# Optimization experiments

Measured on AMD Instinct MI355X. Metric: run time of the kernel, lower is better.

Reference implementation:

```python
import jax, jax.numpy as jnp
import numpy as np

D_MODEL = 512
D_INNER = 2 * D_MODEL      # 1024
DT_RANK = D_MODEL // 16    # 32
D_STATE = 16
D_CONV = 4
NB_LAYERS = 3
BATCH = 64
SEQ = 201
CITY = 200
EPS = 1e-5


def setup_inputs() -> dict:
    key = jax.random.key(0)
    ks = jax.random.split(key, 12)
    def rn(k, shape, scale=0.02):
        return jax.random.normal(k, shape, jnp.float32) * scale
    A_init = jnp.tile(jnp.arange(1, D_STATE + 1, dtype=jnp.float32)[None, None, :],
                      (NB_LAYERS, D_INNER, 1))
    return {
        "x": jax.random.uniform(ks[0], (BATCH, SEQ, 2), jnp.float32),
        "city_count": CITY,
        "embed_W": rn(ks[1], (D_MODEL, 2), 0.5),
        "embed_b": jnp.zeros((D_MODEL,), jnp.float32),
        "norm_w": jnp.ones((NB_LAYERS, D_MODEL), jnp.float32),
        "norm_b": jnp.zeros((NB_LAYERS, D_MODEL), jnp.float32),
        "in_W": rn(ks[2], (NB_LAYERS, 2 * D_INNER, D_MODEL)),
        "conv_w": rn(ks[3], (NB_LAYERS, D_INNER, D_CONV), 0.1),
        "conv_b": jnp.zeros((NB_LAYERS, D_INNER), jnp.float32),
        "xproj_W": rn(ks[4], (NB_LAYERS, DT_RANK + 2 * D_STATE, D_INNER)),
        "dtproj_W": rn(ks[5], (NB_LAYERS, D_INNER, DT_RANK), 0.1),
        "dtproj_b": rn(ks[6], (NB_LAYERS, D_INNER), 0.5),
        "A_log": jnp.log(A_init),
        "Dskip": jnp.ones((NB_LAYERS, D_INNER), jnp.float32),
        "out_W": rn(ks[7], (NB_LAYERS, D_MODEL, D_INNER)),
        "normf_w": jnp.ones((D_MODEL,), jnp.float32),
        "normf_b": jnp.zeros((D_MODEL,), jnp.float32),
        "head_W": rn(ks[8], (CITY, D_MODEL)),
    }


def _silu(v):
    return v * jax.nn.sigmoid(v)


def _layernorm(v, w, b):
    v = v.astype(jnp.float32)
    mu = v.mean(-1, keepdims=True)
    var = ((v - mu) ** 2).mean(-1, keepdims=True)
    return (v - mu) * jax.lax.rsqrt(var + EPS) * w + b


def _rmsnorm(v, w, b):
    v = v.astype(jnp.float32)
    ms = (v * v).mean(-1, keepdims=True)
    return v * jax.lax.rsqrt(ms + EPS) * w + b


def _mamba_mixer(h, in_W, cw, cb, xp_W, dt_W, dt_b, A_log, Dv, o_W):
    B, L, _ = h.shape
    xz = jnp.einsum('bld,ed->ble', h, in_W)              # (B,L,2*di)
    xc, z = jnp.split(xz, 2, axis=-1)
    # causal depthwise conv over time
    xt = xc.transpose(0, 2, 1)                           # (B,di,L)
    xt = jax.lax.conv_general_dilated(
        xt, cw[:, None, :], (1,), [(D_CONV - 1, 0)],
        dimension_numbers=('NCH', 'OIH', 'NCH'),
        feature_group_count=D_INNER)
    u = _silu((xt + cb[None, :, None]).transpose(0, 2, 1))   # (B,L,di)
    x_dbl = jnp.einsum('bld,ed->ble', u, xp_W)
    dt_r = x_dbl[..., :DT_RANK]
    Bm = x_dbl[..., DT_RANK:DT_RANK + D_STATE]
    Cm = x_dbl[..., DT_RANK + D_STATE:]
    dt = jax.nn.softplus(jnp.einsum('blr,dr->bld', dt_r, dt_W) + dt_b)
    A = -jnp.exp(A_log)                                  # (di,n)

    def step(hst, ins):
        dt_t, B_t, C_t, u_t = ins                        # (B,di),(B,n),(B,n),(B,di)
        dA = jnp.exp(dt_t[..., None] * A)                # (B,di,n)
        hst = dA * hst + (dt_t * u_t)[..., None] * B_t[:, None, :]
        y = jnp.einsum('bdn,bn->bd', hst, C_t)
        return hst, y

    h0 = jnp.zeros((B, D_INNER, D_STATE), h.dtype)
    _, ys = jax.lax.scan(step, h0, (dt.transpose(1, 0, 2), Bm.transpose(1, 0, 2),
                                    Cm.transpose(1, 0, 2), u.transpose(1, 0, 2)))
    y = ys.transpose(1, 0, 2) + Dv * u
    y = y * _silu(z)
    return jnp.einsum('bld,ed->ble', y, o_W)


def reference(x, city_count, embed_W, embed_b, norm_w, norm_b, in_W, conv_w, conv_b,
              xproj_W, dtproj_W, dtproj_b, A_log, Dskip, out_W, normf_w, normf_b, head_W):
    h = jnp.einsum('blc,dc->bld', x, embed_W) + embed_b
    residual = None
    for i in range(NB_LAYERS):
        residual = h if residual is None else h + residual   # residual in fp32
        hn = _layernorm(residual, norm_w[i], norm_b[i])
        h = _mamba_mixer(hn, in_W[i], conv_w[i], conv_b[i], xproj_W[i],
                         dtproj_W[i], dtproj_b[i], A_log[i], Dskip[i], out_W[i])
    residual = h + residual
    xf = _rmsnorm(residual, normf_w, normf_b)                # final fused RMSNorm
    logits = jnp.einsum('bld,cd->blc', xf, head_W)           # output head -> city logits
    return logits
```

## Files before the change

### kernel.cpp

```cpp
#include <hip/hip_runtime.h>
#include <hip/hip_fp16.h>
#include <math.h>

#define D_MODEL 512
#define D_INNER 1024
#define DT_RANK 32
#define D_STATE 16
#define D_CONV 4
#define NB_LAYERS 3
#define BATCH 64
#define SEQ 201
#define CITY 200
#define M_ROWS (BATCH * SEQ)
#define M_PAD 12928
#define EPS 1e-5f
#define NCH 8
#define CL 26

typedef __attribute__((ext_vector_type(8))) short short8;
typedef __attribute__((ext_vector_type(8))) unsigned short ushort8;
typedef __attribute__((ext_vector_type(4))) float f32x4;

__device__ __forceinline__ float sigmoidf_(float x) { return 1.f / (1.f + __expf(-x)); }

__device__ __forceinline__ unsigned short f2b(float f) {
  union { float f; unsigned int u; } v; v.f = f;
  unsigned int r = (v.u + 0x7fff + ((v.u >> 16) & 1)) >> 16;
  return (unsigned short)r;
}
__device__ __forceinline__ float b2f(unsigned short h) {
  union { unsigned int u; float f; } v; v.u = ((unsigned int)h) << 16; return v.f;
}
__device__ __forceinline__ unsigned short f2h(float f) {
  __half h = __float2half(f); return *(unsigned short*)&h;
}
__device__ __forceinline__ float h2f(unsigned short u) {
  __half h = *(__half*)&u; return __half2float(h);
}

__device__ __forceinline__ void gload_lds16(const void* g, void* l) {
  __builtin_amdgcn_global_load_lds(
      (const __attribute__((address_space(1))) void*)g,
      (__attribute__((address_space(3))) void*)l, 16, 0, 0);
}

__global__ __launch_bounds__(256) void k_f2b(const float* __restrict__ in,
                                             unsigned short* __restrict__ out,
                                             int n, int n_total) {
  int i = blockIdx.x * 256 + threadIdx.x;
  if (i < n) out[i] = f2b(in[i]);
  else if (i < n_total) out[i] = 0;
}

__global__ __launch_bounds__(256) void k_padW(const float* __restrict__ W,
                                              unsigned short* __restrict__ out,
                                              int rows, int incols, int outcols) {
  int i = blockIdx.x * 256 + threadIdx.x;
  if (i >= rows * outcols) return;
  int n = i / outcols, k = i - n * outcols;
  out[i] = (k < incols) ? f2b(W[(size_t)n * incols + k]) : 0;
}

__global__ __launch_bounds__(256) void k_padR(const float* __restrict__ W,
                                              unsigned short* __restrict__ out,
                                              int nl, int inrows, int outrows, int cols) {
  int i = blockIdx.x * 256 + threadIdx.x;
  if (i >= nl * outrows * cols) return;
  int c = i % cols;
  int r = (i / cols) % outrows;
  int L = i / (cols * outrows);
  out[i] = (r < inrows) ? f2b(W[((size_t)L * inrows + r) * cols + c]) : 0;
}

__global__ __launch_bounds__(256) void k_convT(const float* __restrict__ cw,
                                               float* __restrict__ cwT) {
  int i = blockIdx.x * 256 + threadIdx.x;
  if (i >= NB_LAYERS * D_CONV * D_INNER) return;
  int d = i & (D_INNER - 1);
  int k = (i >> 10) & 3;
  int L = i >> 12;
  cwT[i] = cw[((size_t)L * D_INNER + d) * D_CONV + k];
}

__global__ __launch_bounds__(256) void k_embed(const float* __restrict__ x,
                                               const float* __restrict__ W,
                                               const float* __restrict__ b,
                                               float* __restrict__ h) {
  int idx = blockIdx.x * 256 + threadIdx.x;
  if (idx >= M_ROWS * D_MODEL) return;
  int d = idx & (D_MODEL - 1);
  int m = idx >> 9;
  float x0 = x[m * 2 + 0], x1 = x[m * 2 + 1];
  h[idx] = fmaf(x0, W[d * 2 + 0], fmaf(x1, W[d * 2 + 1], b[d]));
}

__global__ __launch_bounds__(256) void k_resid_norm(const float* __restrict__ h,
                                                    float* __restrict__ resid,
                                                    float* __restrict__ out,
                                                    unsigned short* __restrict__ out_b,
                                                    const float* __restrict__ w,
                                                    const float* __restrict__ b,
                                                    int addRes, int mode) {
  int row = blockIdx.x * 4 + (threadIdx.x >> 6);
  int lane = threadIdx.x & 63;
  if (row >= M_ROWS) return;
  const float* hp = h + (size_t)row * D_MODEL;
  float* rp = resid + (size_t)row * D_MODEL;
  float v[8];
#pragma unroll
  for (int j = 0; j < 8; ++j) {
    float t = hp[j * 64 + lane];
    if (addRes) t += rp[j * 64 + lane];
    v[j] = t;
    rp[j * 64 + lane] = t;
  }
  float mu = 0.f, rstd;
  if (mode == 0) {
    float s = 0.f;
#pragma unroll
    for (int j = 0; j < 8; ++j) s += v[j];
#pragma unroll
    for (int o = 1; o < 64; o <<= 1) s += __shfl_xor(s, o);
    mu = s * (1.f / D_MODEL);
    float vs = 0.f;
#pragma unroll
    for (int j = 0; j < 8; ++j) { float d0 = v[j] - mu; vs += d0 * d0; }
#pragma unroll
    for (int o = 1; o < 64; o <<= 1) vs += __shfl_xor(vs, o);
    rstd = rsqrtf(vs * (1.f / D_MODEL) + EPS);
  } else {
    float s = 0.f;
#pragma unroll
    for (int j = 0; j < 8; ++j) s += v[j] * v[j];
#pragma unroll
    for (int o = 1; o < 64; o <<= 1) s += __shfl_xor(s, o);
    rstd = rsqrtf(s * (1.f / D_MODEL) + EPS);
  }
#pragma unroll
  for (int j = 0; j < 8; ++j) {
    int c = j * 64 + lane;
    float o = (v[j] - mu) * rstd * w[c] + b[c];
    if (out) out[(size_t)row * D_MODEL + c] = o;
    if (out_b) out_b[(size_t)row * D_MODEL + c] = f2b(o);
  }
}

template <int BOUT, int ACT>
__global__ __launch_bounds__(256) void k_gemm_mfma(const unsigned short* __restrict__ A,
                                                   const unsigned short* __restrict__ B,
                                                   const float* __restrict__ bias,
                                                   void* __restrict__ Cv, int ldc,
                                                   int M, int Nout, int K) {
  __shared__ unsigned short lA[2][128 * 64];
  __shared__ unsigned short lB[2][128 * 64];
  int tid = threadIdx.x;
  int wave = tid >> 6, lane = tid & 63;
  int bm = blockIdx.y * 128, bn = blockIdx.x * 128;
  int wm = (wave >> 1) * 64, wn = (wave & 1) * 64;
  f32x4 acc[4][4] = {};

  auto stage = [&](int kt, int bb) {
    int k0 = kt * 64;
#pragma unroll
    for (int i = 0; i < 4; ++i) {
      int e = (i * 256 + tid) * 8;
      int r = e >> 6, c = e & 63;
      gload_lds16(A + (size_t)(bm + r) * K + k0 + c, &lA[bb][e]);
      gload_lds16(B + (size_t)(bn + r) * K + k0 + c, &lB[bb][e]);
    }
  };

  int nk = K >> 6;
  stage(0, 0);
  __syncthreads();
  for (int t = 0; t < nk; ++t) {
    int cur = t & 1;
    if (t + 1 < nk) stage(t + 1, cur ^ 1);
#pragma unroll
    for (int ks = 0; ks < 2; ++ks) {
      int koff = ks * 32 + (lane >> 4) * 8;
      short8 a[4], b[4];
#pragma unroll
      for (int i = 0; i < 4; ++i)
        a[i] = *(const short8*)&lA[cur][(wm + i * 16 + (lane & 15)) * 64 + koff];
#pragma unroll
      for (int j = 0; j < 4; ++j)
        b[j] = *(const short8*)&lB[cur][(wn + j * 16 + (lane & 15)) * 64 + koff];
#pragma unroll
      for (int i = 0; i < 4; ++i)
#pragma unroll
        for (int j = 0; j < 4; ++j)
          acc[i][j] = __builtin_amdgcn_mfma_f32_16x16x32_bf16(a[i], b[j], acc[i][j], 0, 0, 0);
    }
    __syncthreads();
  }
#pragma unroll
  for (int i = 0; i < 4; ++i) {
    int row0 = bm + wm + i * 16 + (lane >> 4) * 4;
#pragma unroll
    for (int j = 0; j < 4; ++j) {
      int col = bn + wn + j * 16 + (lane & 15);
#pragma unroll
      for (int r = 0; r < 4; ++r) {
        int m = row0 + r;
        if (m < M && col < Nout) {
          float v = acc[i][j][r];
          if (ACT) { v += bias[col]; v = (v > 20.f) ? v : __logf(1.f + __expf(v)); }
          if (BOUT == 1) ((unsigned short*)Cv)[(size_t)m * ldc + col] = f2b(v);
          else if (BOUT == 2) ((unsigned short*)Cv)[(size_t)m * ldc + col] = f2h(v);
          else ((float*)Cv)[(size_t)m * ldc + col] = v;
        }
      }
    }
  }
}

__global__ __launch_bounds__(256) void k_conv_silu(const unsigned short* __restrict__ xz,
                                                   const float* __restrict__ cwT,
                                                   const float* __restrict__ cb,
                                                   unsigned short* __restrict__ ub) {
  int i = blockIdx.x * 256 + threadIdx.x;
  if (i >= M_ROWS * 128) return;
  int dg = (i & 127) << 3;
  int m = i >> 7;
  int l = m % SEQ;
  float y[8];
  float4 cb0 = *(const float4*)&cb[dg];
  float4 cb1 = *(const float4*)&cb[dg + 4];
  y[0] = cb0.x; y[1] = cb0.y; y[2] = cb0.z; y[3] = cb0.w;
  y[4] = cb1.x; y[5] = cb1.y; y[6] = cb1.z; y[7] = cb1.w;
#pragma unroll
  for (int k = 0; k < D_CONV; ++k) {
    int ls = l - (D_CONV - 1) + k;
    if (ls >= 0) {
      ushort8 xv = *(const ushort8*)&xz[(size_t)(m - (D_CONV - 1) + k) * 2048 + dg];
      float4 w0 = *(const float4*)&cwT[k * D_INNER + dg];
      float4 w1 = *(const float4*)&cwT[k * D_INNER + dg + 4];
      y[0] = fmaf(w0.x, b2f(xv[0]), y[0]);
      y[1] = fmaf(w0.y, b2f(xv[1]), y[1]);
      y[2] = fmaf(w0.z, b2f(xv[2]), y[2]);
      y[3] = fmaf(w0.w, b2f(xv[3]), y[3]);
      y[4] = fmaf(w1.x, b2f(xv[4]), y[4]);
      y[5] = fmaf(w1.y, b2f(xv[5]), y[5]);
      y[6] = fmaf(w1.z, b2f(xv[6]), y[6]);
      y[7] = fmaf(w1.w, b2f(xv[7]), y[7]);
    }
  }
  ushort8 o;
#pragma unroll
  for (int j = 0; j < 8; ++j) { float v = y[j]; v = v * sigmoidf_(v); o[j] = f2b(v); }
  *(ushort8*)&ub[(size_t)m * D_INNER + dg] = o;
}

__global__ __launch_bounds__(256) void k_scan_p1(const unsigned short* __restrict__ dt,
                                                 const unsigned short* __restrict__ ub,
                                                 const unsigned short* __restrict__ xdb,
                                                 const float* __restrict__ A_log,
                                                 unsigned short* __restrict__ L,
                                                 float* __restrict__ dtsum) {
  int tid = threadIdx.x;
  int b = blockIdx.x >> 3, c = blockIdx.x & 7;
  int d = blockIdx.y * 256 + tid;
  int t0 = c * CL, t1 = t0 + CL < SEQ ? t0 + CL : SEQ;
  float Areg[D_STATE], hst[D_STATE];
#pragma unroll
  for (int n = 0; n < D_STATE; ++n) {
    Areg[n] = -__expf(A_log[d * D_STATE + n]);
    hst[n] = 0.f;
  }
  float ds = 0.f;
  size_t row0 = (size_t)b * SEQ;
  for (int t = t0; t < t1; ++t) {
    size_t m = row0 + t;
    float dtv = h2f(dt[m * D_INNER + d]);
    float uv = b2f(ub[m * D_INNER + d]);
    const unsigned short* xp = xdb + m * 64 + 32;
    ushort8 b0 = *(const ushort8*)&xp[0];
    ushort8 b1 = *(const ushort8*)&xp[8];
    float du = dtv * uv;
    ds += dtv;
#pragma unroll
    for (int j = 0; j < 8; ++j)
      hst[j] = fmaf(__expf(dtv * Areg[j]), hst[j], du * b2f(b0[j]));
#pragma unroll
    for (int j = 0; j < 8; ++j)
      hst[8 + j] = fmaf(__expf(dtv * Areg[8 + j]), hst[8 + j], du * b2f(b1[j]));
  }
  size_t base = ((size_t)(b * NCH + c) * D_INNER + d) * D_STATE;
  ushort8 o0, o1;
#pragma unroll
  for (int j = 0; j < 8; ++j) { o0[j] = f2b(hst[j]); o1[j] = f2b(hst[8 + j]); }
  *(ushort8*)&L[base] = o0;
  *(ushort8*)&L[base + 8] = o1;
  dtsum[(size_t)(b * NCH + c) * D_INNER + d] = ds;
}

__global__ __launch_bounds__(256) void k_scan_fix(const float* __restrict__ A_log,
                                                  const float* __restrict__ dtsum,
                                                  unsigned short* __restrict__ L) {
  int tid = threadIdx.x;
  int b = blockIdx.x;
  int d = blockIdx.y * 256 + tid;
  float Areg[D_STATE], h[D_STATE];
#pragma unroll
  for (int n = 0; n < D_STATE; ++n) {
    Areg[n] = -__expf(A_log[d * D_STATE + n]);
    h[n] = 0.f;
  }
  for (int c = 0; c < NCH; ++c) {
    size_t base = ((size_t)(b * NCH + c) * D_INNER + d) * D_STATE;
    ushort8 l0 = *(const ushort8*)&L[base];
    ushort8 l1 = *(const ushort8*)&L[base + 8];
    float ds = dtsum[(size_t)(b * NCH + c) * D_INNER + d];
    ushort8 o0, o1;
#pragma unroll
    for (int j = 0; j < 8; ++j) { o0[j] = f2b(h[j]); o1[j] = f2b(h[8 + j]); }
    *(ushort8*)&L[base] = o0;
    *(ushort8*)&L[base + 8] = o1;
#pragma unroll
    for (int j = 0; j < 8; ++j)
      h[j] = fmaf(__expf(Areg[j] * ds), h[j], b2f(l0[j]));
#pragma unroll
    for (int j = 0; j < 8; ++j)
      h[8 + j] = fmaf(__expf(Areg[8 + j] * ds), h[8 + j], b2f(l1[j]));
  }
}

__global__ __launch_bounds__(256) void k_scan_p2(const unsigned short* __restrict__ dt,
                                                 const unsigned short* __restrict__ xz,
                                                 const unsigned short* __restrict__ ub,
                                                 const unsigned short* __restrict__ xdb,
                                                 const float* __restrict__ A_log,
                                                 const float* __restrict__ Dv,
                                                 const unsigned short* __restrict__ L,
                                                 unsigned short* __restrict__ yb) {
  int tid = threadIdx.x;
  int b = blockIdx.x >> 3, c = blockIdx.x & 7;
  int d = blockIdx.y * 256 + tid;
  int t0 = c * CL, t1 = t0 + CL < SEQ ? t0 + CL : SEQ;
  float Areg[D_STATE], hst[D_STATE];
  size_t base = ((size_t)(b * NCH + c) * D_INNER + d) * D_STATE;
  ushort8 l0 = *(const ushort8*)&L[base];
  ushort8 l1 = *(const ushort8*)&L[base + 8];
#pragma unroll
  for (int n = 0; n < D_STATE; ++n) Areg[n] = -__expf(A_log[d * D_STATE + n]);
#pragma unroll
  for (int j = 0; j < 8; ++j) { hst[j] = b2f(l0[j]); hst[8 + j] = b2f(l1[j]); }
  float Dd = Dv[d];
  size_t row0 = (size_t)b * SEQ;
  for (int t = t0; t < t1; ++t) {
    size_t m = row0 + t;
    float dtv = h2f(dt[m * D_INNER + d]);
    float uv = b2f(ub[m * D_INNER + d]);
    float zv = b2f(xz[m * 2048 + 1024 + d]);
    const unsigned short* xp = xdb + m * 64 + 32;
    ushort8 b0 = *(const ushort8*)&xp[0];
    ushort8 b1 = *(const ushort8*)&xp[8];
    ushort8 c0 = *(const ushort8*)&xp[16];
    ushort8 c1 = *(const ushort8*)&xp[24];
    float du = dtv * uv;
    float y0 = 0.f, y1 = 0.f, y2 = 0.f, y3 = 0.f;
#pragma unroll
    for (int j = 0; j < 8; ++j) {
      hst[j] = fmaf(__expf(dtv * Areg[j]), hst[j], du * b2f(b0[j]));
      float& yq = (j < 4) ? y0 : y1;
      yq = fmaf(hst[j], b2f(c0[j]), yq);
    }
#pragma unroll
    for (int j = 0; j < 8; ++j) {
      hst[8 + j] = fmaf(__expf(dtv * Areg[8 + j]), hst[8 + j], du * b2f(b1[j]));
      float& yq = (j < 4) ? y2 : y3;
      yq = fmaf(hst[8 + j], b2f(c1[j]), yq);
    }
    float y = (y0 + y1) + (y2 + y3);
    y = fmaf(Dd, uv, y);
    y = y * (zv * sigmoidf_(zv));
    yb[m * D_INNER + d] = f2b(y);
  }
}

extern "C" void kernel_launch(void* const* d_in, const int* in_sizes, int n_in,
                              void* d_out, int out_size, void* d_ws, size_t ws_size,
                              hipStream_t stream) {
  const float* x        = (const float*)d_in[0];
  const float* embed_W  = (const float*)d_in[2];
  const float* embed_b  = (const float*)d_in[3];
  const float* norm_w   = (const float*)d_in[4];
  const float* norm_b   = (const float*)d_in[5];
  const float* in_W     = (const float*)d_in[6];
  const float* conv_w   = (const float*)d_in[7];
  const float* conv_b   = (const float*)d_in[8];
  const float* xproj_W  = (const float*)d_in[9];
  const float* dtproj_W = (const float*)d_in[10];
  const float* dtproj_b = (const float*)d_in[11];
  const float* A_log    = (const float*)d_in[12];
  const float* Dskip    = (const float*)d_in[13];
  const float* out_W    = (const float*)d_in[14];
  const float* normf_w  = (const float*)d_in[15];
  const float* normf_b  = (const float*)d_in[16];
  const float* head_W   = (const float*)d_in[17];
  float* out = (float*)d_out;

  size_t bf16_elems = (size_t)M_ROWS * 2048 + (size_t)M_PAD * 2048 + (size_t)M_PAD * 64 +
                      (size_t)NB_LAYERS * (2048 * 512 + 512 * 1024 + 128 * 1024 + 1024 * 64) +
                      256 * 512;
  size_t need = (size_t)M_ROWS * 1024 * 4 + (size_t)M_ROWS * 1024 * 2 + bf16_elems * 2 +
                (size_t)NB_LAYERS * D_CONV * D_INNER * 4;
  if (ws_size < need) return;

  float* ws = (float*)d_ws;
  float* buf_res  = ws;
  float* buf_h    = buf_res  + (size_t)M_ROWS * 512;
  unsigned short* buf_dt   = (unsigned short*)(buf_h + (size_t)M_ROWS * 512);
  unsigned short* buf_xz   = buf_dt + (size_t)M_ROWS * 1024;
  unsigned short* buf_ub   = buf_xz + (size_t)M_ROWS * 2048;
  unsigned short* buf_yb   = buf_ub + (size_t)M_PAD * 1024;
  unsigned short* buf_hnb  = buf_yb;
  unsigned short* buf_xdb  = buf_yb + (size_t)M_PAD * 1024;
  unsigned short* buf_wib  = buf_xdb + (size_t)M_PAD * 64;
  unsigned short* buf_wob  = buf_wib + (size_t)NB_LAYERS * 2048 * 512;
  unsigned short* buf_wxb  = buf_wob + (size_t)NB_LAYERS * 512 * 1024;
  unsigned short* buf_wdtb = buf_wxb + (size_t)NB_LAYERS * 128 * 1024;
  unsigned short* buf_whb  = buf_wdtb + (size_t)NB_LAYERS * 1024 * 64;
  float* buf_cwT = (float*)(buf_whb + (size_t)256 * 512);

  unsigned short* buf_L = (unsigned short*)buf_h;
  float* buf_dts = (float*)(buf_L + (size_t)BATCH * NCH * D_INNER * D_STATE);

  dim3 blk(256);

  k_f2b<<<(NB_LAYERS * 2048 * 512 + 255) / 256, blk, 0, stream>>>(
      in_W, buf_wib, NB_LAYERS * 2048 * 512, NB_LAYERS * 2048 * 512);
  k_f2b<<<(NB_LAYERS * 512 * 1024 + 255) / 256, blk, 0, stream>>>(
      out_W, buf_wob, NB_LAYERS * 512 * 1024, NB_LAYERS * 512 * 1024);
  k_padR<<<(NB_LAYERS * 128 * 1024 + 255) / 256, blk, 0, stream>>>(
      xproj_W, buf_wxb, NB_LAYERS, 64, 128, 1024);
  k_padW<<<(NB_LAYERS * 1024 * 64 + 255) / 256, blk, 0, stream>>>(
      dtproj_W, buf_wdtb, NB_LAYERS * 1024, DT_RANK, 64);
  k_f2b<<<(256 * 512 + 255) / 256, blk, 0, stream>>>(head_W, buf_whb, CITY * 512, 256 * 512);
  k_convT<<<(NB_LAYERS * D_CONV * D_INNER + 255) / 256, blk, 0, stream>>>(conv_w, buf_cwT);

  k_embed<<<(M_ROWS * D_MODEL + 255) / 256, blk, 0, stream>>>(x, embed_W, embed_b, buf_h);

  for (int i = 0; i < NB_LAYERS; ++i) {
    k_resid_norm<<<(M_ROWS + 3) / 4, blk, 0, stream>>>(
        buf_h, buf_res, nullptr, buf_hnb, norm_w + i * D_MODEL, norm_b + i * D_MODEL,
        i > 0 ? 1 : 0, 0);

    k_gemm_mfma<1, 0><<<dim3(2048 / 128, M_PAD / 128), blk, 0, stream>>>(
        buf_hnb, buf_wib + (size_t)i * 2048 * 512, nullptr, buf_xz, 2048, M_ROWS, 2048, 512);

    k_conv_silu<<<(M_ROWS * 128 + 255) / 256, blk, 0, stream>>>(
        buf_xz, buf_cwT + (size_t)i * D_CONV * D_INNER, conv_b + (size_t)i * D_INNER, buf_ub);

    k_gemm_mfma<1, 0><<<dim3(1, M_PAD / 128), blk, 0, stream>>>(
        buf_ub, buf_wxb + (size_t)i * 128 * 1024, nullptr, buf_xdb, 64, M_ROWS, 64, 1024);

    k_gemm_mfma<2, 1><<<dim3(1024 / 128, M_PAD / 128), blk, 0, stream>>>(
        buf_xdb, buf_wdtb + (size_t)i * 1024 * 64, dtproj_b + (size_t)i * D_INNER,
        buf_dt, 1024, M_ROWS, 1024, 64);

    const float* Ai = A_log + (size_t)i * D_INNER * D_STATE;
    k_scan_p1<<<dim3(BATCH * NCH, D_INNER / 256), blk, 0, stream>>>(
        buf_dt, buf_ub, buf_xdb, Ai, buf_L, buf_dts);
    k_scan_fix<<<dim3(BATCH, D_INNER / 256), blk, 0, stream>>>(Ai, buf_dts, buf_L);
    k_scan_p2<<<dim3(BATCH * NCH, D_INNER / 256), blk, 0, stream>>>(
        buf_dt, buf_xz, buf_ub, buf_xdb, Ai, Dskip + (size_t)i * D_INNER, buf_L, buf_yb);

    k_gemm_mfma<0, 0><<<dim3(512 / 128, M_PAD / 128), blk, 0, stream>>>(
        buf_yb, buf_wob + (size_t)i * 512 * 1024, nullptr, buf_h, 512, M_ROWS, 512, 1024);
  }

  k_resid_norm<<<(M_ROWS + 3) / 4, blk, 0, stream>>>(
      buf_h, buf_res, nullptr, buf_hnb, normf_w, normf_b, 1, 1);

  k_gemm_mfma<0, 0><<<dim3(256 / 128, M_PAD / 128), blk, 0, stream>>>(
      buf_hnb, buf_whb, nullptr, out, CITY, M_ROWS, CITY, 512);
}
```

Measured before the change: 890.0 us.

## Swizzle LDS layout, remap workgroups per XCD, drop double buffering in MFMA GEMM

The GEMM now XOR-swizzles the column offset of each 16-byte chunk by row, both when loading global memory into LDS and when reading MFMA fragments, so row-strided reads avoid LDS bank conflicts. Block IDs are remapped so consecutive tiles land on the same XCD, which should improve L2 reuse. Double-buffered LDS is replaced by a single buffer with a sync after each load, halving LDS use and likely raising occupancy, at the cost of losing the overlap between loads and compute.

```diff
diff --git a/kernel.cpp b/kernel.cpp
--- a/kernel.cpp
+++ b/kernel.cpp
@@ -151,41 +151,44 @@
                                                    const float* __restrict__ bias,
                                                    void* __restrict__ Cv, int ldc,
                                                    int M, int Nout, int K) {
-  __shared__ unsigned short lA[2][128 * 64];
-  __shared__ unsigned short lB[2][128 * 64];
+  __shared__ unsigned short lA[128 * 64];
+  __shared__ unsigned short lB[128 * 64];
   int tid = threadIdx.x;
   int wave = tid >> 6, lane = tid & 63;
-  int bm = blockIdx.y * 128, bn = blockIdx.x * 128;
+  int nx = gridDim.x;
+  int nwg = nx * gridDim.y;
+  int bid = blockIdx.y * nx + blockIdx.x;
+  int q = nwg >> 3, rr = nwg & 7;
+  int xcd = bid & 7, idx = bid >> 3;
+  int swz = (xcd < rr ? xcd * (q + 1) : rr * (q + 1) + (xcd - rr) * q) + idx;
+  int bm = (swz / nx) * 128, bn = (swz % nx) * 128;
   int wm = (wave >> 1) * 64, wn = (wave & 1) * 64;
   f32x4 acc[4][4] = {};
 
-  auto stage = [&](int kt, int bb) {
-    int k0 = kt * 64;
+  for (int k0 = 0; k0 < K; k0 += 64) {
 #pragma unroll
     for (int i = 0; i < 4; ++i) {
       int e = (i * 256 + tid) * 8;
       int r = e >> 6, c = e & 63;
-      gload_lds16(A + (size_t)(bm + r) * K + k0 + c, &lA[bb][e]);
-      gload_lds16(B + (size_t)(bn + r) * K + k0 + c, &lB[bb][e]);
-    }
-  };
-
-  int nk = K >> 6;
-  stage(0, 0);
-  __syncthreads();
-  for (int t = 0; t < nk; ++t) {
-    int cur = t & 1;
-    if (t + 1 < nk) stage(t + 1, cur ^ 1);
+      int csrc = c ^ ((r & 7) << 3);
+      gload_lds16(A + (size_t)(bm + r) * K + k0 + csrc, &lA[e]);
+      gload_lds16(B + (size_t)(bn + r) * K + k0 + csrc, &lB[e]);
+    }
+    __syncthreads();
 #pragma unroll
     for (int ks = 0; ks < 2; ++ks) {
       int koff = ks * 32 + (lane >> 4) * 8;
       short8 a[4], b[4];
 #pragma unroll
-      for (int i = 0; i < 4; ++i)
-        a[i] = *(const short8*)&lA[cur][(wm + i * 16 + (lane & 15)) * 64 + koff];
-#pragma unroll
-      for (int j = 0; j < 4; ++j)
-        b[j] = *(const short8*)&lB[cur][(wn + j * 16 + (lane & 15)) * 64 + koff];
+      for (int i = 0; i < 4; ++i) {
+        int row = wm + i * 16 + (lane & 15);
+        a[i] = *(const short8*)&lA[row * 64 + (koff ^ ((row & 7) << 3))];
+      }
+#pragma unroll
+      for (int j = 0; j < 4; ++j) {
+        int row = wn + j * 16 + (lane & 15);
+        b[j] = *(const short8*)&lB[row * 64 + (koff ^ ((row & 7) << 3))];
+      }
 #pragma unroll
       for (int i = 0; i < 4; ++i)
 #pragma unroll
```

Result: faster. 814.2 us (-8.5%).
